# Kernel optimization log

Measured on AMD Instinct MI355X. Metric: run time of the kernel, lower is better.

Reference implementation:

```python
import jax, jax.numpy as jnp
import numpy as np

EMB = 512          # embedding_size
N_NODES = 16384    # len(nodes)
N_EVENTS = 1_000_000
N_PAIRS = 200_000  # distinct (variant, place) groups


def setup_inputs() -> dict:
    key = jax.random.key(0)
    rng = np.random.default_rng(0)
    embeddings = jax.random.normal(key, (N_NODES, EMB), dtype=jnp.float32)
    pair_place = rng.integers(0, N_NODES, N_PAIRS, dtype=np.int32)   # place id per (variant,place) pair
    event_pair = rng.integers(0, N_PAIRS, N_EVENTS, dtype=np.int32)  # which pair each event belongs to
    event_src = rng.integers(0, N_NODES, N_EVENTS, dtype=np.int32)   # source activity per event
    event_ndst = rng.integers(1, 5, N_EVENTS, dtype=np.int32)        # |next_activities| per event (>=1)
    dst_event = np.repeat(np.arange(N_EVENTS, dtype=np.int32), event_ndst)  # event id per dst entry
    dst_node = rng.integers(0, N_NODES, dst_event.shape[0], dtype=np.int32) # dst activity node ids
    return {
        "embeddings": embeddings,
        "pair_place": jnp.asarray(pair_place),
        "event_pair": jnp.asarray(event_pair),
        "event_src": jnp.asarray(event_src),
        "event_ndst": jnp.asarray(event_ndst),
        "dst_event": jnp.asarray(dst_event),
        "dst_node": jnp.asarray(dst_node),
    }


def reference(embeddings, pair_place, event_pair, event_src, event_ndst, dst_event, dst_node):
    N, E = embeddings.shape
    num_events = event_pair.shape[0]
    num_pairs = pair_place.shape[0]
    # torch.mean(torch.stack(e)) averages over ALL elements of the stacked
    # [k, 1, 3E] concat tensors, so only per-row means of the embeddings matter:
    # mean(cat(place_f, src_f, dst_f)) = (mean(place_f)+mean(src_f)+mean(dst_f))/3.
    node_mean = embeddings.mean(axis=1)  # [N]
    # dst_f = (sum over next_activities of embeddings[dst]) / (n_dst + 1)
    dst_sum = jax.ops.segment_sum(node_mean[dst_node], dst_event, num_segments=num_events)  # [num_events]
    ndst = event_ndst.astype(node_mean.dtype)
    event_place = pair_place[event_pair]
    # per-event scalar = mean over the 3E concat features
    s = (node_mean[event_place] + node_mean[event_src] + dst_sum / (ndst + 1.0)) / 3.0
    # per (variant, place) pair: mean over that pair's events
    pair_sum = jax.ops.segment_sum(s, event_pair, num_segments=num_pairs)
    pair_cnt = jax.ops.segment_sum(jnp.ones_like(s), event_pair, num_segments=num_pairs)
    pair_mean = jnp.where(pair_cnt > 0, pair_sum / jnp.maximum(pair_cnt, 1.0), 0.0)
    # per place: mean over the pairs that touched it (only pairs with >=1 event exist)
    place_sum = jax.ops.segment_sum(pair_mean, pair_place, num_segments=N)
    place_cnt = jax.ops.segment_sum(jnp.where(pair_cnt > 0, 1.0, 0.0).astype(s.dtype), pair_place, num_segments=N)
    place_mean = jnp.where(place_cnt > 0, place_sum / jnp.maximum(place_cnt, 1.0), 0.0)
    # final row is the scalar broadcast across cat_embedding_size = 3*E columns
    return jnp.broadcast_to(place_mean[:, None], (N, 3 * E))
```

## Files before the change

kernel.cpp:

```cpp
#include <hip/hip_runtime.h>
#include <hip/hip_fp16.h>

constexpr int EMB = 512;

typedef float floatx4 __attribute__((ext_vector_type(4)));
typedef unsigned uintx4 __attribute__((ext_vector_type(4)));

constexpr float T_SCALE = 1048576.0f;
constexpr float T_INV_SCALE = 1.0f / 1048576.0f;

__device__ __forceinline__ unsigned pack1_32(float t) {
    int q = __float2int_rn(t * T_SCALE);
    return (unsigned)(q + (1 << 26));
}
__device__ __forceinline__ void unpack32(unsigned a, int& cnt, float& sum) {
    cnt = (int)((a + (1u << 25)) >> 26);
    int q = (int)(a - ((unsigned)cnt << 26));
    sum = (float)q * T_INV_SCALE;
}

constexpr float FP_SCALE = 4194304.0f;
constexpr float FP_INV_SCALE = 1.0f / 4194304.0f;

__device__ __forceinline__ unsigned long long pack1_64(float v) {
    long long q = (long long)__float2int_rn(v * FP_SCALE);
    return (unsigned long long)(q + (1LL << 32));
}
__device__ __forceinline__ void unpack64(unsigned long long p, int& cnt, float& sum) {
    long long t = (long long)p;
    cnt = (int)((t + (1LL << 31)) >> 32);
    long long q = t - ((long long)cnt << 32);
    sum = (float)q * FP_INV_SCALE;
}

__global__ void node_mean_k(const float* __restrict__ emb,
                            float* __restrict__ node_mean,
                            __half* __restrict__ node_mean16,
                            uintx4* __restrict__ zero4, int n_zero4,
                            int n_nodes) {
    int g = blockIdx.x * blockDim.x + threadIdx.x;
    if (g < n_zero4) zero4[g] = (uintx4){0u, 0u, 0u, 0u};
    int gwave = g >> 6;
    int lane = threadIdx.x & 63;
    if (gwave >= n_nodes) return;
    const float4* row = (const float4*)emb + (size_t)gwave * (EMB / 4);
    float4 a = row[lane];
    float4 b = row[lane + 64];
    float s = (a.x + a.y) + (a.z + a.w) + (b.x + b.y) + (b.z + b.w);
#pragma unroll
    for (int off = 32; off > 0; off >>= 1)
        s += __shfl_down(s, off, 64);
    if (lane == 0) {
        float m = s * (1.0f / (float)EMB);
        node_mean[gwave] = m;
        node_mean16[gwave] = __float2half(m);
    }
}

__global__ void event_fused_k(const int* __restrict__ dst_event,
                              const int* __restrict__ dst_node,
                              const int* __restrict__ event_pair,
                              const int* __restrict__ event_src,
                              const __half* __restrict__ nm16,
                              unsigned* __restrict__ pair_acc, int n_dst) {
    int i = blockIdx.x * blockDim.x + threadIdx.x;
    if (i >= n_dst) return;
    int e = dst_event[i];
    if (i > 0 && dst_event[i - 1] == e) return;
    int j1 = i + 1, j2 = i + 2, j3 = i + 3;
    bool b1 = j1 < n_dst, b2 = j2 < n_dst, b3 = j3 < n_dst;
    int e1 = b1 ? dst_event[j1] : -1;
    int e2 = b2 ? dst_event[j2] : -1;
    int e3 = b3 ? dst_event[j3] : -1;
    int d0 = dst_node[i];
    int d1 = b1 ? dst_node[j1] : 0;
    int d2 = b2 ? dst_node[j2] : 0;
    int d3 = b3 ? dst_node[j3] : 0;
    int pr = event_pair[e];
    float sv = __half2float(nm16[event_src[e]]);
    float h0 = __half2float(nm16[d0]);
    float h1 = __half2float(nm16[d1]);
    float h2 = __half2float(nm16[d2]);
    float h3 = __half2float(nm16[d3]);
    bool v1 = (e1 == e), v2 = (e2 == e), v3 = (e3 == e);
    float dsum = h0 + (v1 ? h1 : 0.0f) + (v2 ? h2 : 0.0f) + (v3 ? h3 : 0.0f);
    int nd = 1 + (int)v1 + (int)v2 + (int)v3;
    int j = i + 4;
    while (v3 && j < n_dst && dst_event[j] == e) {
        dsum += __half2float(nm16[dst_node[j]]);
        ++nd; ++j;
    }
    float t = sv + dsum / (float)(nd + 1);
    atomicAdd(&pair_acc[pr], pack1_32(t));
}

__global__ void pair_k(const unsigned* __restrict__ pair_acc,
                       const int* __restrict__ pair_place,
                       const float* __restrict__ node_mean,
                       unsigned long long* __restrict__ place_acc, int n_pairs) {
    int p = blockIdx.x * blockDim.x + threadIdx.x;
    if (p >= n_pairs) return;
    int cnt; float tsum;
    unpack32(pair_acc[p], cnt, tsum);
    if (cnt > 0) {
        int pl = pair_place[p];
        float pm = node_mean[pl] * (1.0f / 3.0f) + tsum / (3.0f * (float)cnt);
        atomicAdd(&place_acc[pl], pack1_64(pm));
    }
}

__global__ void out_k(const unsigned long long* __restrict__ place_acc,
                      float* __restrict__ out) {
    constexpr int ROW_F4 = 3 * EMB / 4;
    int row = blockIdx.x;
    int t = threadIdx.x;
    int cnt; float psum;
    unpack64(place_acc[row], cnt, psum);
    float v = (cnt > 0) ? psum / (float)cnt : 0.0f;
    floatx4 val = {v, v, v, v};
    floatx4* dst = (floatx4*)out + (size_t)row * ROW_F4;
    __builtin_nontemporal_store(val, dst + t);
    if (t < ROW_F4 - 256)
        __builtin_nontemporal_store(val, dst + 256 + t);
}

extern "C" void kernel_launch(void* const* d_in, const int* in_sizes, int n_in,
                              void* d_out, int out_size, void* d_ws, size_t ws_size,
                              hipStream_t stream) {
    const float* emb        = (const float*)d_in[0];
    const int*   pair_place = (const int*)d_in[1];
    const int*   event_pair = (const int*)d_in[2];
    const int*   event_src  = (const int*)d_in[3];
    const int*   dst_event  = (const int*)d_in[5];
    const int*   dst_node   = (const int*)d_in[6];

    const int n_nodes  = in_sizes[0] / EMB;
    const int n_pairs  = in_sizes[1];
    const int n_dst    = in_sizes[5];

    char* base = (char*)d_ws;
    float* node_mean = (float*)base;
    __half* nm16 = (__half*)(base + (size_t)n_nodes * 4);
    unsigned* pair_acc = (unsigned*)(base + (size_t)n_nodes * 6);
    unsigned long long* place_acc =
        (unsigned long long*)(base + (size_t)n_nodes * 6 + (size_t)n_pairs * 4);

    const int n_zero4 = (n_pairs * 4 + n_nodes * 8 + 15) / 16;

    node_mean_k<<<(n_nodes + 3) / 4, 256, 0, stream>>>(
        emb, node_mean, nm16, (uintx4*)pair_acc, n_zero4, n_nodes);
    event_fused_k<<<(n_dst + 255) / 256, 256, 0, stream>>>(
        dst_event, dst_node, event_pair, event_src, nm16, pair_acc, n_dst);
    pair_k<<<(n_pairs + 255) / 256, 256, 0, stream>>>(
        pair_acc, pair_place, node_mean, place_acc, n_pairs);
    out_k<<<n_nodes, 256, 0, stream>>>(place_acc, (float*)d_out);
}
```

Measured before the change: 217.2 us.

## Process four dst entries per thread with vectorized int4 loads in event kernel

Each thread of the event kernel now covers four consecutive dst entries instead of one. It loads eight dst_event and dst_node values with int4 vector loads and handles every event that starts within its quad, reusing the loaded lookahead values. This cuts redundant per-thread reloads of neighbouring indices and reduces thread count, but adds per-thread serial work (up to four events, each with gathers and an atomic) and more branch divergence.

New measurement: 217.6 us. Within noise of the previous version (+0.2%).

```diff
diff --git a/kernel.cpp b/kernel.cpp
--- a/kernel.cpp
+++ b/kernel.cpp
@@ -63,35 +63,52 @@
                               const int* __restrict__ event_src,
                               const __half* __restrict__ nm16,
                               unsigned* __restrict__ pair_acc, int n_dst) {
-    int i = blockIdx.x * blockDim.x + threadIdx.x;
-    if (i >= n_dst) return;
-    int e = dst_event[i];
-    if (i > 0 && dst_event[i - 1] == e) return;
-    int j1 = i + 1, j2 = i + 2, j3 = i + 3;
-    bool b1 = j1 < n_dst, b2 = j2 < n_dst, b3 = j3 < n_dst;
-    int e1 = b1 ? dst_event[j1] : -1;
-    int e2 = b2 ? dst_event[j2] : -1;
-    int e3 = b3 ? dst_event[j3] : -1;
-    int d0 = dst_node[i];
-    int d1 = b1 ? dst_node[j1] : 0;
-    int d2 = b2 ? dst_node[j2] : 0;
-    int d3 = b3 ? dst_node[j3] : 0;
-    int pr = event_pair[e];
-    float sv = __half2float(nm16[event_src[e]]);
-    float h0 = __half2float(nm16[d0]);
-    float h1 = __half2float(nm16[d1]);
-    float h2 = __half2float(nm16[d2]);
-    float h3 = __half2float(nm16[d3]);
-    bool v1 = (e1 == e), v2 = (e2 == e), v3 = (e3 == e);
-    float dsum = h0 + (v1 ? h1 : 0.0f) + (v2 ? h2 : 0.0f) + (v3 ? h3 : 0.0f);
-    int nd = 1 + (int)v1 + (int)v2 + (int)v3;
-    int j = i + 4;
-    while (v3 && j < n_dst && dst_event[j] == e) {
-        dsum += __half2float(nm16[dst_node[j]]);
-        ++nd; ++j;
+    int q = blockIdx.x * blockDim.x + threadIdx.x;
+    int i0 = q << 2;
+    if (i0 >= n_dst) return;
+    int ev[8], nd[8];
+    if (i0 + 8 <= n_dst) {
+        int4 a = *(const int4*)(dst_event + i0);
+        int4 b = *(const int4*)(dst_event + i0 + 4);
+        int4 c = *(const int4*)(dst_node + i0);
+        int4 d = *(const int4*)(dst_node + i0 + 4);
+        ev[0] = a.x; ev[1] = a.y; ev[2] = a.z; ev[3] = a.w;
+        ev[4] = b.x; ev[5] = b.y; ev[6] = b.z; ev[7] = b.w;
+        nd[0] = c.x; nd[1] = c.y; nd[2] = c.z; nd[3] = c.w;
+        nd[4] = d.x; nd[5] = d.y; nd[6] = d.z; nd[7] = d.w;
+    } else {
+#pragma unroll
+        for (int j = 0; j < 8; ++j) {
+            int p = i0 + j;
+            ev[j] = (p < n_dst) ? dst_event[p] : -1;
+            nd[j] = (p < n_dst) ? dst_node[p] : 0;
+        }
     }
-    float t = sv + dsum / (float)(nd + 1);
-    atomicAdd(&pair_acc[pr], pack1_32(t));
+    int prev = (i0 == 0) ? -1 : dst_event[i0 - 1];
+#pragma unroll
+    for (int k = 0; k < 4; ++k) {
+        int e = ev[k];
+        int pr = (k == 0) ? prev : ev[k - 1];
+        if (e < 0 || pr == e) continue;
+        float dsum = __half2float(nm16[nd[k]]);
+        int ndc = 1;
+        if (ev[k + 1] == e) {
+            dsum += __half2float(nm16[nd[k + 1]]); ++ndc;
+            if (ev[k + 2] == e) {
+                dsum += __half2float(nm16[nd[k + 2]]); ++ndc;
+                if (ev[k + 3] == e) {
+                    dsum += __half2float(nm16[nd[k + 3]]); ++ndc;
+                    int j = i0 + k + 4;
+                    while (j < n_dst && dst_event[j] == e) {
+                        dsum += __half2float(nm16[dst_node[j]]);
+                        ++ndc; ++j;
+                    }
+                }
+            }
+        }
+        float t = __half2float(nm16[event_src[e]]) + dsum / (float)(ndc + 1);
+        atomicAdd(&pair_acc[event_pair[e]], pack1_32(t));
+    }
 }
 
 __global__ void pair_k(const unsigned* __restrict__ pair_acc,
@@ -149,7 +166,8 @@
 
     node_mean_k<<<(n_nodes + 3) / 4, 256, 0, stream>>>(
         emb, node_mean, nm16, (uintx4*)pair_acc, n_zero4, n_nodes);
-    event_fused_k<<<(n_dst + 255) / 256, 256, 0, stream>>>(
+    const int n_quads = (n_dst + 3) / 4;
+    event_fused_k<<<(n_quads + 255) / 256, 256, 0, stream>>>(
         dst_event, dst_node, event_pair, event_src, nm16, pair_acc, n_dst);
     pair_k<<<(n_pairs + 255) / 256, 256, 0, stream>>>(
         pair_acc, pair_place, node_mean, place_acc, n_pairs);
```
